# Kernel tuning notes

Measured on AMD Instinct MI355X. Metric: run time of the kernel, lower is better.

## Reference

```python
import jax, jax.numpy as jnp
import numpy as np

B, S, D = 32, 2048, 128
SCALE = 11.313708498984761  # sqrt(128)


def setup_inputs() -> dict:
    key = jax.random.key(0)
    kq, kk, kv = jax.random.split(key, 3)
    q = jax.random.normal(kq, (B, S, D), dtype=jnp.float32)
    k = jax.random.normal(kk, (B, S, D), dtype=jnp.float32)
    v = jax.random.normal(kv, (B, S, D), dtype=jnp.float32)
    # causal mask: True where masked (j > i), broadcast across batch
    causal = jnp.triu(jnp.ones((S, S), dtype=bool), k=1)
    mask = jnp.broadcast_to(causal, (B, S, S))
    return {"q": q, "k": k, "v": v, "mask": mask}


def reference(q, k, v, mask):
    # a = (q @ k^T) / scale, masked_fill(mask, -inf), softmax over keys, a @ v
    a = jnp.einsum("bqd,bkd->bqk", q, k) / SCALE  # [B, S, S]
    a = jnp.where(mask, -jnp.inf, a)
    a = jax.nn.softmax(a, axis=2)
    output = jnp.einsum("bqk,bkd->bqd", a, v)  # [B, S, D]
    return (a, output)
```

## Files before the change

### kernel.cpp

```cpp
#include <hip/hip_runtime.h>
#include <hip/hip_bf16.h>
#include <math.h>


typedef __attribute__((ext_vector_type(8))) short bf16x8;
typedef __attribute__((ext_vector_type(4))) short bf16x4;
typedef __attribute__((ext_vector_type(4))) float f32x4;

#define MFMA(a, b, c) __builtin_amdgcn_mfma_f32_16x16x32_bf16((a), (b), (c), 0, 0, 0)

constexpr int   Sdim  = 2048;
constexpr int   Ddim  = 128;
constexpr int   BATCH = 32;
constexpr int   NT    = Sdim / 64;
constexpr float INV_SCALE = 0.08838834764831845f;
constexpr float NEG_BIG   = -1e30f;
constexpr int   KPAD = 8;
constexpr int   PADV = 8;
constexpr int   PADP = 8;

__device__ __forceinline__ void bar_lds() {
    asm volatile("s_waitcnt lgkmcnt(0)\n\ts_barrier" ::: "memory");
}

__device__ __forceinline__ bf16x8 pack8(const float* p) {
    float4 a = *(const float4*)p;
    float4 b = *(const float4*)(p + 4);
    union { __hip_bfloat16 h[8]; bf16x8 v; } u;
    u.h[0] = __float2bfloat16(a.x); u.h[1] = __float2bfloat16(a.y);
    u.h[2] = __float2bfloat16(a.z); u.h[3] = __float2bfloat16(a.w);
    u.h[4] = __float2bfloat16(b.x); u.h[5] = __float2bfloat16(b.y);
    u.h[6] = __float2bfloat16(b.z); u.h[7] = __float2bfloat16(b.w);
    return u.v;
}

__device__ __forceinline__ bf16x4 pack4(float4 a) {
    union { __hip_bfloat16 h[4]; bf16x4 v; } u;
    u.h[0] = __float2bfloat16(a.x); u.h[1] = __float2bfloat16(a.y);
    u.h[2] = __float2bfloat16(a.z); u.h[3] = __float2bfloat16(a.w);
    return u.v;
}

__global__ __launch_bounds__(256, 2)
void attn_kernel(const float* __restrict__ qg,
                 const float* __restrict__ kg,
                 const float* __restrict__ vg,
                 float* __restrict__ a_out,
                 float* __restrict__ o_out)
{
    const int jb   = blockIdx.x;
    const int b    = blockIdx.y;
    const int tid  = threadIdx.x;
    const int wave = tid >> 6;
    const int lane = tid & 63;
    const int li   = lane & 15;
    const int quad = lane >> 4;

    __shared__ __hip_bfloat16 kl[64][Ddim + KPAD];
    __shared__ __hip_bfloat16 vt[Ddim][64 + PADV];
    __shared__ __hip_bfloat16 pt[64][64 + PADP];

    const size_t boff = (size_t)b * Sdim * Ddim;
    const float* qb = qg + boff;
    const float* kb = kg + boff;
    const float* vb = vg + boff;
    float* ab = a_out + (size_t)b * Sdim * Sdim;

    for (int sel = 0; sel < 2; ++sel) {
        const int qi   = sel ? (NT - 1 - jb) : jb;
        const int q0   = qi * 64;
        const int row0 = q0 + wave * 16;

        bf16x8 qf[4];
        {
            const float* qrow = qb + (size_t)(row0 + li) * Ddim + quad * 8;
            #pragma unroll
            for (int ks = 0; ks < 4; ++ks)
                qf[ks] = pack8(qrow + ks * 32);
        }

        {
            const int c0  = (qi + 1) * 64;
            const int zc4 = (Sdim - c0) >> 2;
            const f32x4 z = (f32x4){0.f, 0.f, 0.f, 0.f};
            for (int rr = 0; rr < 16; ++rr) {
                f32x4* dst = (f32x4*)(ab + (size_t)(row0 + rr) * Sdim + c0);
                for (int c = lane; c < zc4; c += 64)
                    __builtin_nontemporal_store(z, dst + c);
            }
        }

        float m[4], l[4];
        #pragma unroll
        for (int r = 0; r < 4; ++r) { m[r] = NEG_BIG; l[r] = 0.f; }

        for (int kt = 0; kt <= qi; ++kt) {
            const int kv0 = kt * 64;

            bar_lds();
            {
                const float* kbt = kb + (size_t)kv0 * Ddim;
                int idx = tid;
                #pragma unroll
                for (int it = 0; it < 8; ++it, idx += 256) {
                    const int kk = idx >> 5;
                    const int d0 = (idx & 31) * 4;
                    *(bf16x4*)&kl[kk][d0] = pack4(*(const float4*)(kbt + (size_t)kk * Ddim + d0));
                }
            }
            bar_lds();

            f32x4 acc[4];
            #pragma unroll
            for (int t = 0; t < 4; ++t) acc[t] = (f32x4){0.f, 0.f, 0.f, 0.f};
            #pragma unroll
            for (int t = 0; t < 4; ++t)
                #pragma unroll
                for (int ks = 0; ks < 4; ++ks) {
                    bf16x8 kf = *(const bf16x8*)&kl[t * 16 + li][ks * 32 + quad * 8];
                    acc[t] = MFMA(qf[ks], kf, acc[t]);
                }

            float s[4][4];
            #pragma unroll
            for (int t = 0; t < 4; ++t)
                #pragma unroll
                for (int r = 0; r < 4; ++r) {
                    float sv = acc[t][r] * INV_SCALE;
                    if (kt == qi) {
                        int col = kv0 + t * 16 + li;
                        int row = row0 + quad * 4 + r;
                        if (col > row) sv = NEG_BIG;
                    }
                    s[t][r] = sv;
                }

            #pragma unroll
            for (int r = 0; r < 4; ++r) {
                float tm = fmaxf(fmaxf(s[0][r], s[1][r]), fmaxf(s[2][r], s[3][r]));
                #pragma unroll
                for (int off = 1; off < 16; off <<= 1)
                    tm = fmaxf(tm, __shfl_xor(tm, off, 64));
                float mn    = fmaxf(m[r], tm);
                float alpha = __expf(m[r] - mn);
                float se = __expf(s[0][r] - mn) + __expf(s[1][r] - mn)
                         + __expf(s[2][r] - mn) + __expf(s[3][r] - mn);
                #pragma unroll
                for (int off = 1; off < 16; off <<= 1)
                    se += __shfl_xor(se, off, 64);
                l[r] = l[r] * alpha + se;
                m[r] = mn;
            }
        }

        float invl[4];
        #pragma unroll
        for (int r = 0; r < 4; ++r) invl[r] = 1.0f / l[r];

        f32x4 oacc[8];
        #pragma unroll
        for (int n = 0; n < 8; ++n) oacc[n] = (f32x4){0.f, 0.f, 0.f, 0.f};

        for (int kt = 0; kt <= qi; ++kt) {
            const int kv0 = kt * 64;

            bar_lds();
            {
                const float* kbt = kb + (size_t)kv0 * Ddim;
                const float* vbt = vb + (size_t)kv0 * Ddim;
                int idx = tid;
                #pragma unroll
                for (int it = 0; it < 8; ++it, idx += 256) {
                    const int kk = idx >> 5;
                    const int d0 = (idx & 31) * 4;
                    *(bf16x4*)&kl[kk][d0] = pack4(*(const float4*)(kbt + (size_t)kk * Ddim + d0));
                }
                idx = tid;
                #pragma unroll
                for (int it = 0; it < 8; ++it, idx += 256) {
                    const int kk = idx >> 5;
                    const int d0 = (idx & 31) * 4;
                    float4 vv = *(const float4*)(vbt + (size_t)kk * Ddim + d0);
                    vt[d0 + 0][kk] = __float2bfloat16(vv.x);
                    vt[d0 + 1][kk] = __float2bfloat16(vv.y);
                    vt[d0 + 2][kk] = __float2bfloat16(vv.z);
                    vt[d0 + 3][kk] = __float2bfloat16(vv.w);
                }
            }
            bar_lds();

            f32x4 acc[4];
            #pragma unroll
            for (int t = 0; t < 4; ++t) acc[t] = (f32x4){0.f, 0.f, 0.f, 0.f};
            #pragma unroll
            for (int t = 0; t < 4; ++t)
                #pragma unroll
                for (int ks = 0; ks < 4; ++ks) {
                    bf16x8 kf = *(const bf16x8*)&kl[t * 16 + li][ks * 32 + quad * 8];
                    acc[t] = MFMA(qf[ks], kf, acc[t]);
                }

            #pragma unroll
            for (int r = 0; r < 4; ++r) {
                const int rowL = wave * 16 + quad * 4 + r;
                float* dst = ab + (size_t)(q0 + rowL) * Sdim + kv0 + li;
                #pragma unroll
                for (int t = 0; t < 4; ++t) {
                    float sv = acc[t][r] * INV_SCALE;
                    if (kt == qi && (kv0 + t * 16 + li) > (q0 + rowL)) sv = NEG_BIG;
                    float p = __expf(sv - m[r]) * invl[r];
                    pt[rowL][t * 16 + li] = __float2bfloat16(p);
                    __builtin_nontemporal_store(p, dst + t * 16);
                }
            }

            asm volatile("s_waitcnt lgkmcnt(0)" ::: "memory");

            #pragma unroll
            for (int ks = 0; ks < 2; ++ks) {
                bf16x8 pf = *(const bf16x8*)&pt[wave * 16 + li][ks * 32 + quad * 8];
                #pragma unroll
                for (int nt = 0; nt < 8; ++nt) {
                    bf16x8 vf = *(const bf16x8*)&vt[nt * 16 + li][ks * 32 + quad * 8];
                    oacc[nt] = MFMA(pf, vf, oacc[nt]);
                }
            }
        }

        float* ob = o_out + ((size_t)b * Sdim + row0) * Ddim;
        #pragma unroll
        for (int n = 0; n < 8; ++n)
            #pragma unroll
            for (int r = 0; r < 4; ++r)
                __builtin_nontemporal_store(oacc[n][r],
                    ob + (size_t)(quad * 4 + r) * Ddim + n * 16 + li);
    }
}

extern "C" void kernel_launch(void* const* d_in, const int* in_sizes, int n_in,
                              void* d_out, int out_size, void* d_ws, size_t ws_size,
                              hipStream_t stream)
{
    const float* q = (const float*)d_in[0];
    const float* k = (const float*)d_in[1];
    const float* v = (const float*)d_in[2];

    float* a = (float*)d_out;
    float* o = a + (size_t)BATCH * Sdim * Sdim;

    dim3 grid(NT / 2, BATCH);
    attn_kernel<<<grid, 256, 0, stream>>>(q, k, v, a, o);
}
```

Before: 1.048 ms.

## Prefetch next K/V tile into registers, remap blocks per XCD, raise MFMA priority

Global loads for the next K (and V) tile are issued into registers right after the current tile is written to LDS, so load latency overlaps with the MFMA and softmax work of the current tile. The grid is flattened and remapped so that all blocks of one batch land on the same XCD, with the aim of improving L2 reuse of K/V. s_setprio is raised around the MFMA sections. The prefetch buffers add register pressure under launch_bounds(256,2), which could cause spills.

```diff
diff --git a/kernel.cpp b/kernel.cpp
--- a/kernel.cpp
+++ b/kernel.cpp
@@ -48,8 +48,12 @@
                  float* __restrict__ a_out,
                  float* __restrict__ o_out)
 {
-    const int jb   = blockIdx.x;
-    const int b    = blockIdx.y;
+    const int flat = blockIdx.x;
+    const int xcd  = flat & 7;
+    const int rdec = flat >> 3;
+    const int jb   = rdec & 15;
+    const int b    = xcd + 8 * (rdec >> 4);
+
     const int tid  = threadIdx.x;
     const int wave = tid >> 6;
     const int lane = tid & 63;
@@ -65,6 +69,14 @@
     const float* kb = kg + boff;
     const float* vb = vg + boff;
     float* ab = a_out + (size_t)b * Sdim * Sdim;
+
+    int skk[8], sd0[8];
+    #pragma unroll
+    for (int it = 0; it < 8; ++it) {
+        const int idx = tid + it * 256;
+        skk[it] = idx >> 5;
+        sd0[it] = (idx & 31) * 4;
+    }
 
     for (int sel = 0; sel < 2; ++sel) {
         const int qi   = sel ? (NT - 1 - jb) : jb;
@@ -94,25 +106,30 @@
         #pragma unroll
         for (int r = 0; r < 4; ++r) { m[r] = NEG_BIG; l[r] = 0.f; }
 
+        float4 kpre[8];
+        #pragma unroll
+        for (int it = 0; it < 8; ++it)
+            kpre[it] = *(const float4*)(kb + (size_t)skk[it] * Ddim + sd0[it]);
+
         for (int kt = 0; kt <= qi; ++kt) {
+            bar_lds();
+            #pragma unroll
+            for (int it = 0; it < 8; ++it)
+                *(bf16x4*)&kl[skk[it]][sd0[it]] = pack4(kpre[it]);
+            bar_lds();
+
+            if (kt < qi) {
+                const float* kbt = kb + (size_t)(kt + 1) * 64 * Ddim;
+                #pragma unroll
+                for (int it = 0; it < 8; ++it)
+                    kpre[it] = *(const float4*)(kbt + (size_t)skk[it] * Ddim + sd0[it]);
+            }
+
             const int kv0 = kt * 64;
-
-            bar_lds();
-            {
-                const float* kbt = kb + (size_t)kv0 * Ddim;
-                int idx = tid;
-                #pragma unroll
-                for (int it = 0; it < 8; ++it, idx += 256) {
-                    const int kk = idx >> 5;
-                    const int d0 = (idx & 31) * 4;
-                    *(bf16x4*)&kl[kk][d0] = pack4(*(const float4*)(kbt + (size_t)kk * Ddim + d0));
-                }
-            }
-            bar_lds();
-
             f32x4 acc[4];
             #pragma unroll
             for (int t = 0; t < 4; ++t) acc[t] = (f32x4){0.f, 0.f, 0.f, 0.f};
+            __builtin_amdgcn_s_setprio(1);
             #pragma unroll
             for (int t = 0; t < 4; ++t)
                 #pragma unroll
@@ -120,6 +137,7 @@
                     bf16x8 kf = *(const bf16x8*)&kl[t * 16 + li][ks * 32 + quad * 8];
                     acc[t] = MFMA(qf[ks], kf, acc[t]);
                 }
+            __builtin_amdgcn_s_setprio(0);
 
             float s[4][4];
             #pragma unroll
@@ -161,37 +179,45 @@
         #pragma unroll
         for (int n = 0; n < 8; ++n) oacc[n] = (f32x4){0.f, 0.f, 0.f, 0.f};
 
+        float4 vpre[8];
+        #pragma unroll
+        for (int it = 0; it < 8; ++it) {
+            kpre[it] = *(const float4*)(kb + (size_t)skk[it] * Ddim + sd0[it]);
+            vpre[it] = *(const float4*)(vb + (size_t)skk[it] * Ddim + sd0[it]);
+        }
+
         for (int kt = 0; kt <= qi; ++kt) {
             const int kv0 = kt * 64;
 
             bar_lds();
-            {
-                const float* kbt = kb + (size_t)kv0 * Ddim;
-                const float* vbt = vb + (size_t)kv0 * Ddim;
-                int idx = tid;
-                #pragma unroll
-                for (int it = 0; it < 8; ++it, idx += 256) {
-                    const int kk = idx >> 5;
-                    const int d0 = (idx & 31) * 4;
-                    *(bf16x4*)&kl[kk][d0] = pack4(*(const float4*)(kbt + (size_t)kk * Ddim + d0));
-                }
-                idx = tid;
-                #pragma unroll
-                for (int it = 0; it < 8; ++it, idx += 256) {
-                    const int kk = idx >> 5;
-                    const int d0 = (idx & 31) * 4;
-                    float4 vv = *(const float4*)(vbt + (size_t)kk * Ddim + d0);
-                    vt[d0 + 0][kk] = __float2bfloat16(vv.x);
-                    vt[d0 + 1][kk] = __float2bfloat16(vv.y);
-                    vt[d0 + 2][kk] = __float2bfloat16(vv.z);
-                    vt[d0 + 3][kk] = __float2bfloat16(vv.w);
-                }
-            }
-            bar_lds();
+            #pragma unroll
+            for (int it = 0; it < 8; ++it)
+                *(bf16x4*)&kl[skk[it]][sd0[it]] = pack4(kpre[it]);
+            #pragma unroll
+            for (int it = 0; it < 8; ++it) {
+                const int kk = skk[it], d0 = sd0[it];
+                float4 vv = vpre[it];
+                vt[d0 + 0][kk] = __float2bfloat16(vv.x);
+                vt[d0 + 1][kk] = __float2bfloat16(vv.y);
+                vt[d0 + 2][kk] = __float2bfloat16(vv.z);
+                vt[d0 + 3][kk] = __float2bfloat16(vv.w);
+            }
+            bar_lds();
+
+            if (kt < qi) {
+                const float* kbt = kb + (size_t)(kt + 1) * 64 * Ddim;
+                const float* vbt = vb + (size_t)(kt + 1) * 64 * Ddim;
+                #pragma unroll
+                for (int it = 0; it < 8; ++it) {
+                    kpre[it] = *(const float4*)(kbt + (size_t)skk[it] * Ddim + sd0[it]);
+                    vpre[it] = *(const float4*)(vbt + (size_t)skk[it] * Ddim + sd0[it]);
+                }
+            }
 
             f32x4 acc[4];
             #pragma unroll
             for (int t = 0; t < 4; ++t) acc[t] = (f32x4){0.f, 0.f, 0.f, 0.f};
+            __builtin_amdgcn_s_setprio(1);
             #pragma unroll
             for (int t = 0; t < 4; ++t)
                 #pragma unroll
@@ -199,6 +225,7 @@
                     bf16x8 kf = *(const bf16x8*)&kl[t * 16 + li][ks * 32 + quad * 8];
                     acc[t] = MFMA(qf[ks], kf, acc[t]);
                 }
+            __builtin_amdgcn_s_setprio(0);
 
             #pragma unroll
             for (int r = 0; r < 4; ++r) {
@@ -216,6 +243,7 @@
 
             asm volatile("s_waitcnt lgkmcnt(0)" ::: "memory");
 
+            __builtin_amdgcn_s_setprio(1);
             #pragma unroll
             for (int ks = 0; ks < 2; ++ks) {
                 bf16x8 pf = *(const bf16x8*)&pt[wave * 16 + li][ks * 32 + quad * 8];
@@ -225,6 +253,7 @@
                     oacc[nt] = MFMA(pf, vf, oacc[nt]);
                 }
             }
+            __builtin_amdgcn_s_setprio(0);
         }
 
         float* ob = o_out + ((size_t)b * Sdim + row0) * Ddim;
@@ -248,6 +277,5 @@
     float* a = (float*)d_out;
     float* o = a + (size_t)BATCH * Sdim * Sdim;
 
-    dim3 grid(NT / 2, BATCH);
-    attn_kernel<<<grid, 256, 0, stream>>>(q, k, v, a, o);
-}
+    attn_kernel<<<dim3(512), 256, 0, stream>>>(q, k, v, a, o);
+}
```

Measured after the change: 1.043 ms. No clear change (-0.5%).
